# Optimization experiments

Measured on AMD Instinct MI355X. Metric: run time of the kernel, lower is better.

## Reference

```python
import jax, jax.numpy as jnp
import numpy as np

B, W, H, C = 8, 32, 32, 64   # batch, width, height, hidden_size
NH = 8                        # num_attention_heads
M = 32                        # max_position_embeddings
P = C // 2                    # position_embedding_size (query_positional_score=True)


def setup_inputs() -> dict:
    key = jax.random.key(0)
    ks = jax.random.split(key, 7)
    s = 0.02
    return {
        "hidden_states": jax.random.normal(ks[0], (B, W, H, C), dtype=jnp.float32),
        "row_emb": jax.random.normal(ks[1], (2 * M - 1, P), dtype=jnp.float32) * s,
        "col_emb": jax.random.normal(ks[2], (2 * M - 1, P), dtype=jnp.float32) * s,
        "Wq": jax.random.normal(ks[3], (NH * C, C), dtype=jnp.float32) * s,
        "bq": jnp.zeros((NH * C,), dtype=jnp.float32),
        "Wk": jax.random.normal(ks[4], (NH * C, C), dtype=jnp.float32) * s,
        "bk": jnp.zeros((NH * C,), dtype=jnp.float32),
        "Wv": jax.random.normal(ks[5], (C, NH * C), dtype=jnp.float32) * s,
        "bv": jnp.zeros((C,), dtype=jnp.float32),
    }


def reference(hidden_states, row_emb, col_emb, Wq, bq, Wk, bk, Wv, bv):
    b, w, h, c = hidden_states.shape
    nh = Wq.shape[0] // c
    half = c // 2
    center = row_emb.shape[0] // 2  # = max_position_embeddings - 1

    # projections: all_head_size = nh * c (per source: hidden_size * num_heads)
    q = (hidden_states @ Wq.T + bq).reshape(b, w, h, nh, c)
    k = (hidden_states @ Wk.T + bk).reshape(b, w, h, nh, c)

    # relative index tables: rel[i, j] = (j - i) + (M - 1)
    iw = jnp.arange(w)
    ih = jnp.arange(h)
    rel_w = iw[None, :] - iw[:, None] + center   # (w, w)
    rel_h = ih[None, :] - ih[:, None] + center   # (h, h)
    r_emb = row_emb[rel_w]  # (w, w, P)
    c_emb = col_emb[rel_h]  # (h, h, P)

    # positional scores: q split into row/col halves
    q_row = q[..., :half]
    q_col = q[..., half:]
    row_scores = jnp.einsum('bijhd,ikd->bijhk', q_row, r_emb)  # (b,w,h,nh,w)
    col_scores = jnp.einsum('bijhd,jld->bijhl', q_col, c_emb)  # (b,w,h,nh,h)
    scale = jnp.sqrt(jnp.asarray(c, dtype=hidden_states.dtype))
    scores = (row_scores[..., :, None] + col_scores[..., None, :]) / scale  # (b,w,h,nh,w,h)

    # content scores q^T k
    scores = scores + jnp.einsum('bijhd,bklhd->bijhkl', q, k) / scale

    # softmax over merged spatial key dims (k,l)
    probs = jax.nn.softmax(scores.reshape(b, w, h, nh, w * h), axis=-1).reshape(scores.shape)

    # value mixing directly with hidden_states, then output projection
    mixed = jnp.einsum('bijhkl,bkld->bijhd', probs, hidden_states).reshape(b, w, h, nh * c)
    return mixed @ Wv.T + bv
```

## Files before the change

kernel.cpp:

```cpp
#include <hip/hip_runtime.h>
#include <math.h>

typedef __bf16 bf16;
typedef bf16 bf16x2 __attribute__((ext_vector_type(2)));
typedef bf16 bf16x4 __attribute__((ext_vector_type(4)));
typedef bf16 bf16x8 __attribute__((ext_vector_type(8)));
typedef float f32x4 __attribute__((ext_vector_type(4)));

constexpr int CENTER = 31;
constexpr float QSCALE = 0.125f * 1.4426950408889634f;

static __device__ __forceinline__ unsigned short f2bf_bits(float f) {
    bf16 b = (bf16)f;
    return __builtin_bit_cast(unsigned short, b);
}

static __device__ __forceinline__ float fast_exp2(float x) {
#if __has_builtin(__builtin_amdgcn_exp2f)
    return __builtin_amdgcn_exp2f(x);
#else
    return exp2f(x);
#endif
}

__global__ __launch_bounds__(256)
void prep_qkproj_kernel(const float* __restrict__ hid,
                        const float* __restrict__ Wq, const float* __restrict__ bq,
                        const float* __restrict__ Wk, const float* __restrict__ bk,
                        const float* __restrict__ Wv,
                        bf16* __restrict__ qb, bf16* __restrict__ kb,
                        bf16* __restrict__ htb, bf16* __restrict__ Wvp)
{
    const int id = blockIdx.x;
    const int t  = threadIdx.x;

    if (id >= 512) {
        __shared__ __attribute__((aligned(16))) bf16 hs[64][72];
        const int pb = id - 512;
        const int b  = pb >> 4, kc = pb & 15;

        {
            int row = t >> 2, c4 = (t & 3) * 16;
            const float4* src = (const float4*)(hid + ((size_t)b * 1024 + kc * 64 + row) * 64 + c4);
            bf16 tmp[16];
            #pragma unroll
            for (int u = 0; u < 4; ++u) {
                float4 v = src[u];
                tmp[4*u+0] = (bf16)v.x; tmp[4*u+1] = (bf16)v.y;
                tmp[4*u+2] = (bf16)v.z; tmp[4*u+3] = (bf16)v.w;
            }
            *(int4*)&hs[row][c4]     = ((int4*)tmp)[0];
            *(int4*)&hs[row][c4 + 8] = ((int4*)tmp)[1];
        }
        {
            int idx = pb * 256 + t;
            if (idx < 8192) {
                float4 vv = ((const float4*)Wv)[idx];
                ushort4 pv;
                pv.x = f2bf_bits(vv.x); pv.y = f2bf_bits(vv.y);
                pv.z = f2bf_bits(vv.z); pv.w = f2bf_bits(vv.w);
                int c = idx >> 7, o4 = (idx & 127) * 4;
                size_t dst = (size_t)((c >> 4) * 16 + (o4 >> 5)) * 512 + (c & 15) * 32 + (o4 & 31);
                *(ushort4*)(Wvp + dst) = pv;
            }
        }
        __syncthreads();
        {
            int d = t >> 2, p0 = (t & 3) * 16;
            ushort tmp[16];
            #pragma unroll
            for (int i = 0; i < 16; ++i)
                tmp[i] = __builtin_bit_cast(unsigned short, hs[p0 + i][d]);
            bf16* dst = htb + ((size_t)b * 64 + d) * 1024 + kc * 64 + p0;
            *(int4*)dst       = ((int4*)tmp)[0];
            *(int4*)(dst + 8) = ((int4*)tmp)[1];
        }
        return;
    }

    __shared__ __attribute__((aligned(16))) bf16 As[128][72];
    __shared__ __attribute__((aligned(16))) bf16 Bs[128][72];

    const int pt = id & 63;
    const int ot = (id >> 6) & 3;
    const int z  = (id >> 8) & 1;
    const int p0 = pt * 128;
    const int b  = p0 >> 10;

    const float* Wsrc  = z ? Wk : Wq;
    const float* bias  = z ? bk : bq;
    bf16* outp         = z ? kb : qb;
    const float scale  = z ? 1.0f : QSCALE;

    {
        int row = t >> 1, ch = (t & 1) * 32;
        const float4* asrc = (const float4*)(hid + (size_t)(p0 + row) * 64 + ch);
        const float4* bsrc = (const float4*)(Wsrc + (size_t)(ot * 128 + row) * 64 + ch);
        bf16 ta[32], tb[32];
        #pragma unroll
        for (int u = 0; u < 8; ++u) {
            float4 va = asrc[u], vb = bsrc[u];
            ta[4*u+0] = (bf16)va.x; ta[4*u+1] = (bf16)va.y;
            ta[4*u+2] = (bf16)va.z; ta[4*u+3] = (bf16)va.w;
            tb[4*u+0] = (bf16)vb.x; tb[4*u+1] = (bf16)vb.y;
            tb[4*u+2] = (bf16)vb.z; tb[4*u+3] = (bf16)vb.w;
        }
        #pragma unroll
        for (int u = 0; u < 4; ++u) {
            *(int4*)&As[row][ch + u * 8] = ((int4*)ta)[u];
            *(int4*)&Bs[row][ch + u * 8] = ((int4*)tb)[u];
        }
    }
    __syncthreads();

    const int w = t >> 6, ln = t & 63, l15 = ln & 15, quad = ln >> 4;

    bf16x8 a[2][2];
    #pragma unroll
    for (int mt = 0; mt < 2; ++mt) {
        a[mt][0] = *(const bf16x8*)&As[w * 32 + mt * 16 + l15][quad * 8];
        a[mt][1] = *(const bf16x8*)&As[w * 32 + mt * 16 + l15][32 + quad * 8];
    }

    const f32x4 z4 = {0.f, 0.f, 0.f, 0.f};
    f32x4 acc[2][8];
    #pragma unroll
    for (int mt = 0; mt < 2; ++mt)
        #pragma unroll
        for (int nt = 0; nt < 8; ++nt) acc[mt][nt] = z4;

    #pragma unroll
    for (int nt = 0; nt < 8; ++nt) {
        bf16x8 b0 = *(const bf16x8*)&Bs[nt * 16 + l15][quad * 8];
        bf16x8 b1 = *(const bf16x8*)&Bs[nt * 16 + l15][32 + quad * 8];
        #pragma unroll
        for (int mt = 0; mt < 2; ++mt) {
            acc[mt][nt] = __builtin_amdgcn_mfma_f32_16x16x32_bf16(a[mt][0], b0, acc[mt][nt], 0, 0, 0);
            acc[mt][nt] = __builtin_amdgcn_mfma_f32_16x16x32_bf16(a[mt][1], b1, acc[mt][nt], 0, 0, 0);
        }
    }

    #pragma unroll
    for (int nt = 0; nt < 8; ++nt) {
        int o = ot * 128 + nt * 16 + l15;
        float bv = bias[o];
        int hh = o >> 6, d = o & 63;
        #pragma unroll
        for (int mt = 0; mt < 2; ++mt)
            #pragma unroll
            for (int r = 0; r < 4; ++r) {
                int pos = (p0 & 1023) + w * 32 + mt * 16 + quad * 4 + r;
                float val = (acc[mt][nt][r] + bv) * scale;
                outp[(((size_t)b * 8 + hh) * 1024 + pos) * 64 + d] = (bf16)val;
            }
    }
}

__global__ __launch_bounds__(256)
void bias_kernel(const bf16* __restrict__ qb,
                 const float* __restrict__ row_emb, const float* __restrict__ col_emb,
                 bf16* __restrict__ rowbias, bf16* __restrict__ colbias)
{
    __shared__ __attribute__((aligned(16))) bf16 embRs[63][40];
    __shared__ __attribute__((aligned(16))) bf16 embCs[63][40];

    const int t  = threadIdx.x;
    const int bh = blockIdx.x;
    const int sg = blockIdx.y;

    for (int i = t; i < 2016; i += 256) embRs[i >> 5][i & 31] = (bf16)row_emb[i];
    for (int i = t; i < 2016; i += 256) embCs[i >> 5][i & 31] = (bf16)col_emb[i];
    __syncthreads();

    const int w = t >> 6, ln = t & 63, l15 = ln & 15, quad = ln >> 4;

    #pragma unroll
    for (int u = 0; u < 2; ++u) {
        int s = sg * 8 + u * 4 + w;
        bool cm = s >= 32;
        int ij = cm ? s - 32 : s;

        bf16x8 a[2];
        #pragma unroll
        for (int mt = 0; mt < 2; ++mt) {
            const bf16* ap = cm
                ? qb + ((size_t)bh * 1024 + (mt * 16 + l15) * 32 + ij) * 64 + 32 + quad * 8
                : qb + ((size_t)bh * 1024 + ij * 32 + mt * 16 + l15) * 64 + quad * 8;
            a[mt] = *(const bf16x8*)ap;
        }
        bf16* ob = cm ? colbias : rowbias;

        #pragma unroll
        for (int nt = 0; nt < 2; ++nt) {
            int erow = nt * 16 + l15 + CENTER - ij;
            bf16x8 bfrag = cm ? *(const bf16x8*)&embCs[erow][quad * 8]
                              : *(const bf16x8*)&embRs[erow][quad * 8];
            #pragma unroll
            for (int mt = 0; mt < 2; ++mt) {
                f32x4 c = {0.f, 0.f, 0.f, 0.f};
                c = __builtin_amdgcn_mfma_f32_16x16x32_bf16(a[mt], bfrag, c, 0, 0, 0);
                #pragma unroll
                for (int r = 0; r < 4; ++r) {
                    int ql = mt * 16 + quad * 4 + r;
                    int qrow = cm ? ql * 32 + ij : ij * 32 + ql;
                    ob[((size_t)bh * 1024 + qrow) * 32 + nt * 16 + l15] = (bf16)c[r];
                }
            }
        }
    }
}

__global__ __launch_bounds__(256, 2)
void attn_kernel(const bf16* __restrict__ qb, const bf16* __restrict__ kb,
                 const bf16* __restrict__ htb,
                 const bf16* __restrict__ rowbias, const bf16* __restrict__ colbias,
                 bf16* __restrict__ mixedb)
{
    __shared__ __attribute__((aligned(16))) bf16 Ks[2][64][72];
    __shared__ __attribute__((aligned(16))) bf16 Hts[2][64][72];
    __shared__ __attribute__((aligned(16))) bf16 Pp[4][32][72];

    const int t  = threadIdx.x;
    const int id = blockIdx.x;
    const int r8 = id & 7;
    const int g  = id >> 3;
    const int qt = g & 7;
    const int bh = r8 * 8 + (g >> 3);
    const int b  = bh >> 3, h = bh & 7;
    const int q0 = qt * 128;
    const int w = t >> 6, ln = t & 63, l15 = ln & 15, quad = ln >> 4;

    bf16x8 bq_[2][2];
    float  cbv[2][2][4];
    const bf16* rbp[2];
    #pragma unroll
    for (int mt = 0; mt < 2; ++mt) {
        int qrow = q0 + w * 32 + mt * 16 + l15;
        const bf16* qp = qb + ((size_t)bh * 1024 + qrow) * 64;
        bq_[mt][0] = *(const bf16x8*)(qp + quad * 8);
        bq_[mt][1] = *(const bf16x8*)(qp + 32 + quad * 8);
        #pragma unroll
        for (int par = 0; par < 2; ++par) {
            bf16x4 cv = *(const bf16x4*)(colbias + ((size_t)bh * 1024 + qrow) * 32 + par * 16 + quad * 4);
            #pragma unroll
            for (int r = 0; r < 4; ++r) cbv[mt][par][r] = (float)cv[r];
        }
        rbp[mt] = rowbias + ((size_t)bh * 1024 + qrow) * 32;
    }

    const f32x4 z4 = {0.f, 0.f, 0.f, 0.f};
    f32x4 oacc[2][4];
    float lsum[2] = {0.f, 0.f};
    #pragma unroll
    for (int mt = 0; mt < 2; ++mt)
        #pragma unroll
        for (int dt = 0; dt < 4; ++dt) oacc[mt][dt] = z4;

    bf16* Pw = &Pp[w][0][0];
    const bf16* kcbase = kb + (size_t)bh * 1024 * 64;
    const bf16* hcbase = htb + (size_t)b * 64 * 1024;

    const int srow = t >> 2, sc = (t & 3) << 4;
    const bf16* kptr = kcbase + (size_t)srow * 64 + sc;
    const bf16* hptr = hcbase + (size_t)srow * 1024 + sc;

    int4 kr0 = *(const int4*)(kptr);
    int4 kr1 = *(const int4*)(kptr + 8);
    int4 hr0 = *(const int4*)(hptr);
    int4 hr1 = *(const int4*)(hptr + 8);
    *(int4*)&Ks[0][srow][sc]       = kr0;
    *(int4*)&Ks[0][srow][sc + 8]   = kr1;
    *(int4*)&Hts[0][srow][sc]      = hr0;
    *(int4*)&Hts[0][srow][sc + 8]  = hr1;
    kr0 = *(const int4*)(kptr + 4096);
    kr1 = *(const int4*)(kptr + 4096 + 8);
    hr0 = *(const int4*)(hptr + 64);
    hr1 = *(const int4*)(hptr + 64 + 8);
    bf16x2 rnext[2];
    #pragma unroll
    for (int mt = 0; mt < 2; ++mt) rnext[mt] = *(const bf16x2*)(rbp[mt]);
    __syncthreads();

    int cur = 0;
    for (int kc = 0; kc < 16; ++kc) {
        if (kc < 15) {
            *(int4*)&Ks[cur ^ 1][srow][sc]      = kr0;
            *(int4*)&Ks[cur ^ 1][srow][sc + 8]  = kr1;
            *(int4*)&Hts[cur ^ 1][srow][sc]     = hr0;
            *(int4*)&Hts[cur ^ 1][srow][sc + 8] = hr1;
        }
        float rb[2][2];
        #pragma unroll
        for (int mt = 0; mt < 2; ++mt) {
            rb[mt][0] = (float)rnext[mt][0];
            rb[mt][1] = (float)rnext[mt][1];
        }
        if (kc < 14) {
            const bf16* kn = kptr + (size_t)(kc + 2) * 4096;
            const bf16* hn = hptr + (size_t)(kc + 2) * 64;
            kr0 = *(const int4*)(kn);
            kr1 = *(const int4*)(kn + 8);
            hr0 = *(const int4*)(hn);
            hr1 = *(const int4*)(hn + 8);
        }
        if (kc < 15) {
            #pragma unroll
            for (int mt = 0; mt < 2; ++mt)
                rnext[mt] = *(const bf16x2*)(rbp[mt] + (kc + 1) * 2);
        }

        const bf16 (* __restrict__ Kc)[72]  = Ks[cur];
        const bf16 (* __restrict__ Hc)[72]  = Hts[cur];
        f32x4 sf[2][4];
        #pragma unroll
        for (int mt = 0; mt < 2; ++mt)
            #pragma unroll
            for (int kt = 0; kt < 4; ++kt) {
                float rbv = rb[mt][kt >> 1];
                #pragma unroll
                for (int r = 0; r < 4; ++r)
                    sf[mt][kt][r] = rbv + cbv[mt][kt & 1][r];
            }
        __builtin_amdgcn_s_setprio(1);
        #pragma unroll
        for (int kt = 0; kt < 4; ++kt) {
            bf16x8 aK0 = *(const bf16x8*)&Kc[kt * 16 + l15][quad * 8];
            bf16x8 aK1 = *(const bf16x8*)&Kc[kt * 16 + l15][32 + quad * 8];
            #pragma unroll
            for (int mt = 0; mt < 2; ++mt) {
                sf[mt][kt] = __builtin_amdgcn_mfma_f32_16x16x32_bf16(aK0, bq_[mt][0], sf[mt][kt], 0, 0, 0);
                sf[mt][kt] = __builtin_amdgcn_mfma_f32_16x16x32_bf16(aK1, bq_[mt][1], sf[mt][kt], 0, 0, 0);
            }
        }
        __builtin_amdgcn_s_setprio(0);

        #pragma unroll
        for (int mt = 0; mt < 2; ++mt)
            #pragma unroll
            for (int kt = 0; kt < 4; ++kt) {
                ushort4 pk;
                float p0 = fast_exp2(sf[mt][kt][0]);
                float p1 = fast_exp2(sf[mt][kt][1]);
                float p2 = fast_exp2(sf[mt][kt][2]);
                float p3 = fast_exp2(sf[mt][kt][3]);
                lsum[mt] += (p0 + p1) + (p2 + p3);
                pk.x = f2bf_bits(p0); pk.y = f2bf_bits(p1);
                pk.z = f2bf_bits(p2); pk.w = f2bf_bits(p3);
                *(ushort4*)&Pw[(mt * 16 + l15) * 72 + kt * 16 + quad * 4] = pk;
            }

        bf16x8 bp[2][2];
        #pragma unroll
        for (int mt = 0; mt < 2; ++mt) {
            bp[mt][0] = *(const bf16x8*)&Pw[(mt * 16 + l15) * 72 + quad * 8];
            bp[mt][1] = *(const bf16x8*)&Pw[(mt * 16 + l15) * 72 + 32 + quad * 8];
        }
        __builtin_amdgcn_s_setprio(1);
        #pragma unroll
        for (int dt = 0; dt < 4; ++dt) {
            bf16x8 aH0 = *(const bf16x8*)&Hc[dt * 16 + l15][quad * 8];
            bf16x8 aH1 = *(const bf16x8*)&Hc[dt * 16 + l15][32 + quad * 8];
            #pragma unroll
            for (int mt = 0; mt < 2; ++mt) {
                oacc[mt][dt] = __builtin_amdgcn_mfma_f32_16x16x32_bf16(aH0, bp[mt][0], oacc[mt][dt], 0, 0, 0);
                oacc[mt][dt] = __builtin_amdgcn_mfma_f32_16x16x32_bf16(aH1, bp[mt][1], oacc[mt][dt], 0, 0, 0);
            }
        }
        __builtin_amdgcn_s_setprio(0);

        __syncthreads();
        cur ^= 1;
    }

    float inv[2];
    #pragma unroll
    for (int mt = 0; mt < 2; ++mt) {
        float v = lsum[mt];
        v += __shfl_xor(v, 16);
        v += __shfl_xor(v, 32);
        inv[mt] = 1.0f / v;
    }
    #pragma unroll
    for (int mt = 0; mt < 2; ++mt) {
        int pos = q0 + w * 32 + mt * 16 + l15;
        bf16* mb = mixedb + ((size_t)b * 1024 + pos) * 512 + h * 64;
        #pragma unroll
        for (int dt = 0; dt < 4; ++dt) {
            ushort4 pk;
            pk.x = f2bf_bits(oacc[mt][dt][0] * inv[mt]);
            pk.y = f2bf_bits(oacc[mt][dt][1] * inv[mt]);
            pk.z = f2bf_bits(oacc[mt][dt][2] * inv[mt]);
            pk.w = f2bf_bits(oacc[mt][dt][3] * inv[mt]);
            *(ushort4*)(mb + dt * 16 + quad * 4) = pk;
        }
    }
}

__global__ __launch_bounds__(256)
void out_proj_kernel(const bf16* __restrict__ mixedb,
                     const bf16* __restrict__ Wvp, const float* __restrict__ bv,
                     float* __restrict__ out)
{
    const int t  = threadIdx.x;
    const int p0 = blockIdx.x * 32;
    const int w = t >> 6, ln = t & 63, l15 = ln & 15, quad = ln >> 4;

    float bvv = bv[w * 16 + l15];
    f32x4 acc[2] = {(f32x4){bvv, bvv, bvv, bvv}, (f32x4){bvv, bvv, bvv, bvv}};

    const bf16* arow0 = mixedb + (size_t)(p0 + l15) * 512 + quad * 8;
    const bf16* arow1 = mixedb + (size_t)(p0 + 16 + l15) * 512 + quad * 8;
    const bf16* bbase = Wvp + (size_t)w * 16 * 512 + l15 * 32 + quad * 8;

    #pragma unroll
    for (int kc = 0; kc < 16; ++kc) {
        bf16x8 a0 = *(const bf16x8*)(arow0 + kc * 32);
        bf16x8 a1 = *(const bf16x8*)(arow1 + kc * 32);
        bf16x8 bfrag = *(const bf16x8*)(bbase + kc * 512);
        acc[0] = __builtin_amdgcn_mfma_f32_16x16x32_bf16(a0, bfrag, acc[0], 0, 0, 0);
        acc[1] = __builtin_amdgcn_mfma_f32_16x16x32_bf16(a1, bfrag, acc[1], 0, 0, 0);
    }

    #pragma unroll
    for (int mt = 0; mt < 2; ++mt)
        #pragma unroll
        for (int r = 0; r < 4; ++r)
            out[(size_t)(p0 + mt * 16 + quad * 4 + r) * 64 + w * 16 + l15] = acc[mt][r];
}

extern "C" void kernel_launch(void* const* d_in, const int* in_sizes, int n_in,
                              void* d_out, int out_size, void* d_ws, size_t ws_size,
                              hipStream_t stream)
{
    const float* hid     = (const float*)d_in[0];
    const float* row_emb = (const float*)d_in[1];
    const float* col_emb = (const float*)d_in[2];
    const float* Wq      = (const float*)d_in[3];
    const float* bq      = (const float*)d_in[4];
    const float* Wk      = (const float*)d_in[5];
    const float* bk      = (const float*)d_in[6];
    const float* Wv      = (const float*)d_in[7];
    const float* bv      = (const float*)d_in[8];
    float* out = (float*)d_out;

    bf16* qb      = (bf16*)d_ws;
    bf16* kb      = qb + (size_t)64 * 1024 * 64;
    bf16* htb     = kb + (size_t)64 * 1024 * 64;
    bf16* rowbias = htb + (size_t)8 * 64 * 1024;
    bf16* colbias = rowbias + (size_t)64 * 1024 * 32;
    bf16* mixedb  = colbias + (size_t)64 * 1024 * 32;
    bf16* Wvp     = mixedb + (size_t)8 * 1024 * 512;

    prep_qkproj_kernel<<<640, 256, 0, stream>>>(hid, Wq, bq, Wk, bk, Wv, qb, kb, htb, Wvp);
    bias_kernel<<<dim3(64, 8), 256, 0, stream>>>(qb, row_emb, col_emb, rowbias, colbias);
    attn_kernel<<<512, 256, 0, stream>>>(qb, kb, htb, rowbias, colbias, mixedb);
    out_proj_kernel<<<256, 256, 0, stream>>>(mixedb, Wvp, bv, out);
}
```

Measured before the change: 128.0 us.

## Split attention work across 8 waves with one 16-row query tile each

The attention kernel now launches 512 threads per block instead of 256, and each wave handles 16 query rows instead of 32. The K/H staging loads shrink to one 16-byte load per thread, and per-wave registers (accumulators, Q fragments, biases) are halved. The aim is more resident waves to hide LDS and global latency, at the cost of each K/H tile being reused by fewer MFMAs per wave and more waves contending at each barrier.

Result: slower. 156.7 us (+22.5%).

```diff
diff --git a/kernel.cpp b/kernel.cpp
--- a/kernel.cpp
+++ b/kernel.cpp
@@ -210,7 +210,7 @@
     }
 }
 
-__global__ __launch_bounds__(256, 2)
+__global__ __launch_bounds__(512, 4)
 void attn_kernel(const bf16* __restrict__ qb, const bf16* __restrict__ kb,
                  const bf16* __restrict__ htb,
                  const bf16* __restrict__ rowbias, const bf16* __restrict__ colbias,
@@ -218,7 +218,7 @@
 {
     __shared__ __attribute__((aligned(16))) bf16 Ks[2][64][72];
     __shared__ __attribute__((aligned(16))) bf16 Hts[2][64][72];
-    __shared__ __attribute__((aligned(16))) bf16 Pp[4][32][72];
+    __shared__ __attribute__((aligned(16))) bf16 Pp[8][16][72];
 
     const int t  = threadIdx.x;
     const int id = blockIdx.x;
@@ -230,141 +230,100 @@
     const int q0 = qt * 128;
     const int w = t >> 6, ln = t & 63, l15 = ln & 15, quad = ln >> 4;
 
-    bf16x8 bq_[2][2];
-    float  cbv[2][2][4];
-    const bf16* rbp[2];
-    #pragma unroll
-    for (int mt = 0; mt < 2; ++mt) {
-        int qrow = q0 + w * 32 + mt * 16 + l15;
-        const bf16* qp = qb + ((size_t)bh * 1024 + qrow) * 64;
-        bq_[mt][0] = *(const bf16x8*)(qp + quad * 8);
-        bq_[mt][1] = *(const bf16x8*)(qp + 32 + quad * 8);
-        #pragma unroll
-        for (int par = 0; par < 2; ++par) {
-            bf16x4 cv = *(const bf16x4*)(colbias + ((size_t)bh * 1024 + qrow) * 32 + par * 16 + quad * 4);
-            #pragma unroll
-            for (int r = 0; r < 4; ++r) cbv[mt][par][r] = (float)cv[r];
-        }
-        rbp[mt] = rowbias + ((size_t)bh * 1024 + qrow) * 32;
-    }
-
-    const f32x4 z4 = {0.f, 0.f, 0.f, 0.f};
-    f32x4 oacc[2][4];
-    float lsum[2] = {0.f, 0.f};
-    #pragma unroll
-    for (int mt = 0; mt < 2; ++mt)
-        #pragma unroll
-        for (int dt = 0; dt < 4; ++dt) oacc[mt][dt] = z4;
-
-    bf16* Pw = &Pp[w][0][0];
     const bf16* kcbase = kb + (size_t)bh * 1024 * 64;
     const bf16* hcbase = htb + (size_t)b * 64 * 1024;
 
-    const int srow = t >> 2, sc = (t & 3) << 4;
+    const int srow = t >> 3, sc = (t & 7) * 8;
     const bf16* kptr = kcbase + (size_t)srow * 64 + sc;
     const bf16* hptr = hcbase + (size_t)srow * 1024 + sc;
 
-    int4 kr0 = *(const int4*)(kptr);
-    int4 kr1 = *(const int4*)(kptr + 8);
-    int4 hr0 = *(const int4*)(hptr);
-    int4 hr1 = *(const int4*)(hptr + 8);
-    *(int4*)&Ks[0][srow][sc]       = kr0;
-    *(int4*)&Ks[0][srow][sc + 8]   = kr1;
-    *(int4*)&Hts[0][srow][sc]      = hr0;
-    *(int4*)&Hts[0][srow][sc + 8]  = hr1;
-    kr0 = *(const int4*)(kptr + 4096);
-    kr1 = *(const int4*)(kptr + 4096 + 8);
-    hr0 = *(const int4*)(hptr + 64);
-    hr1 = *(const int4*)(hptr + 64 + 8);
-    bf16x2 rnext[2];
-    #pragma unroll
-    for (int mt = 0; mt < 2; ++mt) rnext[mt] = *(const bf16x2*)(rbp[mt]);
+    int4 kr = *(const int4*)(kptr);
+    int4 hr = *(const int4*)(hptr);
+
+    const int qrow = q0 + w * 16 + l15;
+    const bf16* qp = qb + ((size_t)bh * 1024 + qrow) * 64;
+    bf16x8 bq0 = *(const bf16x8*)(qp + quad * 8);
+    bf16x8 bq1 = *(const bf16x8*)(qp + 32 + quad * 8);
+
+    float cbv[2][4];
+    #pragma unroll
+    for (int par = 0; par < 2; ++par) {
+        bf16x4 cv = *(const bf16x4*)(colbias + ((size_t)bh * 1024 + qrow) * 32 + par * 16 + quad * 4);
+        #pragma unroll
+        for (int r = 0; r < 4; ++r) cbv[par][r] = (float)cv[r];
+    }
+    const bf16* rbp = rowbias + ((size_t)bh * 1024 + qrow) * 32;
+
+    const f32x4 z4 = {0.f, 0.f, 0.f, 0.f};
+    f32x4 oacc[4];
+    float lsum = 0.f;
+    #pragma unroll
+    for (int dt = 0; dt < 4; ++dt) oacc[dt] = z4;
+
+    bf16* Pw = &Pp[w][0][0];
+
+    *(int4*)&Ks[0][srow][sc]  = kr;
+    *(int4*)&Hts[0][srow][sc] = hr;
+    kr = *(const int4*)(kptr + 4096);
+    hr = *(const int4*)(hptr + 64);
+    bf16x2 rnext = *(const bf16x2*)(rbp);
     __syncthreads();
 
     int cur = 0;
     for (int kc = 0; kc < 16; ++kc) {
         if (kc < 15) {
-            *(int4*)&Ks[cur ^ 1][srow][sc]      = kr0;
-            *(int4*)&Ks[cur ^ 1][srow][sc + 8]  = kr1;
-            *(int4*)&Hts[cur ^ 1][srow][sc]     = hr0;
-            *(int4*)&Hts[cur ^ 1][srow][sc + 8] = hr1;
-        }
-        float rb[2][2];
-        #pragma unroll
-        for (int mt = 0; mt < 2; ++mt) {
-            rb[mt][0] = (float)rnext[mt][0];
-            rb[mt][1] = (float)rnext[mt][1];
-        }
+            *(int4*)&Ks[cur ^ 1][srow][sc]  = kr;
+            *(int4*)&Hts[cur ^ 1][srow][sc] = hr;
+        }
+        float rb0 = (float)rnext[0], rb1 = (float)rnext[1];
         if (kc < 14) {
-            const bf16* kn = kptr + (size_t)(kc + 2) * 4096;
-            const bf16* hn = hptr + (size_t)(kc + 2) * 64;
-            kr0 = *(const int4*)(kn);
-            kr1 = *(const int4*)(kn + 8);
-            hr0 = *(const int4*)(hn);
-            hr1 = *(const int4*)(hn + 8);
-        }
-        if (kc < 15) {
+            kr = *(const int4*)(kptr + (size_t)(kc + 2) * 4096);
+            hr = *(const int4*)(hptr + (size_t)(kc + 2) * 64);
+        }
+        if (kc < 15) rnext = *(const bf16x2*)(rbp + (kc + 1) * 2);
+
+        const bf16 (* __restrict__ Kc)[72] = Ks[cur];
+        const bf16 (* __restrict__ Hc)[72] = Hts[cur];
+        f32x4 sf[4];
+        #pragma unroll
+        for (int kt = 0; kt < 4; ++kt) {
+            float rbv = (kt >> 1) ? rb1 : rb0;
             #pragma unroll
-            for (int mt = 0; mt < 2; ++mt)
-                rnext[mt] = *(const bf16x2*)(rbp[mt] + (kc + 1) * 2);
-        }
-
-        const bf16 (* __restrict__ Kc)[72]  = Ks[cur];
-        const bf16 (* __restrict__ Hc)[72]  = Hts[cur];
-        f32x4 sf[2][4];
-        #pragma unroll
-        for (int mt = 0; mt < 2; ++mt)
-            #pragma unroll
-            for (int kt = 0; kt < 4; ++kt) {
-                float rbv = rb[mt][kt >> 1];
-                #pragma unroll
-                for (int r = 0; r < 4; ++r)
-                    sf[mt][kt][r] = rbv + cbv[mt][kt & 1][r];
-            }
+            for (int r = 0; r < 4; ++r)
+                sf[kt][r] = rbv + cbv[kt & 1][r];
+        }
         __builtin_amdgcn_s_setprio(1);
         #pragma unroll
         for (int kt = 0; kt < 4; ++kt) {
             bf16x8 aK0 = *(const bf16x8*)&Kc[kt * 16 + l15][quad * 8];
             bf16x8 aK1 = *(const bf16x8*)&Kc[kt * 16 + l15][32 + quad * 8];
-            #pragma unroll
-            for (int mt = 0; mt < 2; ++mt) {
-                sf[mt][kt] = __builtin_amdgcn_mfma_f32_16x16x32_bf16(aK0, bq_[mt][0], sf[mt][kt], 0, 0, 0);
-                sf[mt][kt] = __builtin_amdgcn_mfma_f32_16x16x32_bf16(aK1, bq_[mt][1], sf[mt][kt], 0, 0, 0);
-            }
+            sf[kt] = __builtin_amdgcn_mfma_f32_16x16x32_bf16(aK0, bq0, sf[kt], 0, 0, 0);
+            sf[kt] = __builtin_amdgcn_mfma_f32_16x16x32_bf16(aK1, bq1, sf[kt], 0, 0, 0);
         }
         __builtin_amdgcn_s_setprio(0);
 
         #pragma unroll
-        for (int mt = 0; mt < 2; ++mt)
-            #pragma unroll
-            for (int kt = 0; kt < 4; ++kt) {
-                ushort4 pk;
-                float p0 = fast_exp2(sf[mt][kt][0]);
-                float p1 = fast_exp2(sf[mt][kt][1]);
-                float p2 = fast_exp2(sf[mt][kt][2]);
-                float p3 = fast_exp2(sf[mt][kt][3]);
-                lsum[mt] += (p0 + p1) + (p2 + p3);
-                pk.x = f2bf_bits(p0); pk.y = f2bf_bits(p1);
-                pk.z = f2bf_bits(p2); pk.w = f2bf_bits(p3);
-                *(ushort4*)&Pw[(mt * 16 + l15) * 72 + kt * 16 + quad * 4] = pk;
-            }
-
-        bf16x8 bp[2][2];
-        #pragma unroll
-        for (int mt = 0; mt < 2; ++mt) {
-            bp[mt][0] = *(const bf16x8*)&Pw[(mt * 16 + l15) * 72 + quad * 8];
-            bp[mt][1] = *(const bf16x8*)&Pw[(mt * 16 + l15) * 72 + 32 + quad * 8];
-        }
+        for (int kt = 0; kt < 4; ++kt) {
+            ushort4 pk;
+            float p0 = fast_exp2(sf[kt][0]);
+            float p1 = fast_exp2(sf[kt][1]);
+            float p2 = fast_exp2(sf[kt][2]);
+            float p3 = fast_exp2(sf[kt][3]);
+            lsum += (p0 + p1) + (p2 + p3);
+            pk.x = f2bf_bits(p0); pk.y = f2bf_bits(p1);
+            pk.z = f2bf_bits(p2); pk.w = f2bf_bits(p3);
+            *(ushort4*)&Pw[l15 * 72 + kt * 16 + quad * 4] = pk;
+        }
+
+        bf16x8 bp0 = *(const bf16x8*)&Pw[l15 * 72 + quad * 8];
+        bf16x8 bp1 = *(const bf16x8*)&Pw[l15 * 72 + 32 + quad * 8];
         __builtin_amdgcn_s_setprio(1);
         #pragma unroll
         for (int dt = 0; dt < 4; ++dt) {
             bf16x8 aH0 = *(const bf16x8*)&Hc[dt * 16 + l15][quad * 8];
             bf16x8 aH1 = *(const bf16x8*)&Hc[dt * 16 + l15][32 + quad * 8];
-            #pragma unroll
-            for (int mt = 0; mt < 2; ++mt) {
-                oacc[mt][dt] = __builtin_amdgcn_mfma_f32_16x16x32_bf16(aH0, bp[mt][0], oacc[mt][dt], 0, 0, 0);
-                oacc[mt][dt] = __builtin_amdgcn_mfma_f32_16x16x32_bf16(aH1, bp[mt][1], oacc[mt][dt], 0, 0, 0);
-            }
+            oacc[dt] = __builtin_amdgcn_mfma_f32_16x16x32_bf16(aH0, bp0, oacc[dt], 0, 0, 0);
+            oacc[dt] = __builtin_amdgcn_mfma_f32_16x16x32_bf16(aH1, bp1, oacc[dt], 0, 0, 0);
         }
         __builtin_amdgcn_s_setprio(0);
 
@@ -372,25 +331,20 @@
         cur ^= 1;
     }
 
-    float inv[2];
-    #pragma unroll
-    for (int mt = 0; mt < 2; ++mt) {
-        float v = lsum[mt];
-        v += __shfl_xor(v, 16);
-        v += __shfl_xor(v, 32);
-        inv[mt] = 1.0f / v;
-    }
-    #pragma unroll
-    for (int mt = 0; mt < 2; ++mt) {
-        int pos = q0 + w * 32 + mt * 16 + l15;
-        bf16* mb = mixedb + ((size_t)b * 1024 + pos) * 512 + h * 64;
+    float v = lsum;
+    v += __shfl_xor(v, 16);
+    v += __shfl_xor(v, 32);
+    float inv = 1.0f / v;
+
+    {
+        bf16* mb = mixedb + ((size_t)b * 1024 + qrow) * 512 + h * 64;
         #pragma unroll
         for (int dt = 0; dt < 4; ++dt) {
             ushort4 pk;
-            pk.x = f2bf_bits(oacc[mt][dt][0] * inv[mt]);
-            pk.y = f2bf_bits(oacc[mt][dt][1] * inv[mt]);
-            pk.z = f2bf_bits(oacc[mt][dt][2] * inv[mt]);
-            pk.w = f2bf_bits(oacc[mt][dt][3] * inv[mt]);
+            pk.x = f2bf_bits(oacc[dt][0] * inv);
+            pk.y = f2bf_bits(oacc[dt][1] * inv);
+            pk.z = f2bf_bits(oacc[dt][2] * inv);
+            pk.w = f2bf_bits(oacc[dt][3] * inv);
             *(ushort4*)(mb + dt * 16 + quad * 4) = pk;
         }
     }
@@ -453,6 +407,6 @@
 
     prep_qkproj_kernel<<<640, 256, 0, stream>>>(hid, Wq, bq, Wk, bk, Wv, qb, kb, htb, Wvp);
     bias_kernel<<<dim3(64, 8), 256, 0, stream>>>(qb, row_emb, col_emb, rowbias, colbias);
-    attn_kernel<<<512, 256, 0, stream>>>(qb, kb, htb, rowbias, colbias, mixedb);
+    attn_kernel<<<512, 512, 0, stream>>>(qb, kb, htb, rowbias, colbias, mixedb);
     out_proj_kernel<<<256, 256, 0, stream>>>(mixedb, Wvp, bv, out);
 }
```
